# Performance work log

Measured on AMD Instinct MI355X. Metric: run time of the kernel, lower is better.

## Reference

```python
import jax, jax.numpy as jnp
import numpy as np

HEADS = 8
DIM_HEAD = 64
SCALE = DIM_HEAD ** -0.5

def layernorm_ch(x, g, eps=1e-5):
    # channel-wise LayerNorm over dim=1 (NCHW), biased variance
    mean = jnp.mean(x, axis=1, keepdims=True)
    var = jnp.var(x, axis=1, keepdims=True)
    return (x - mean) * jax.lax.rsqrt(var + eps) * g[None, :, None, None]

def setup_inputs() -> dict:
    key = jax.random.key(0)
    ks = jax.random.split(key, 4)
    B, C, H, W = 16, 512, 64, 64
    hidden = HEADS * DIM_HEAD
    x = jax.random.normal(ks[0], (B, C, H, W), dtype=jnp.float32)
    w_qkv = jax.random.normal(ks[1], (3 * hidden, C), dtype=jnp.float32) * (C ** -0.5)
    w_out = jax.random.normal(ks[2], (C, hidden), dtype=jnp.float32) * (hidden ** -0.5)
    b_out = jnp.zeros((C,), dtype=jnp.float32)
    g_out = jnp.ones((C,), dtype=jnp.float32)
    g_ln = jnp.ones((C,), dtype=jnp.float32)
    return {"x": x, "w_qkv": w_qkv, "w_out": w_out, "b_out": b_out, "g_out": g_out, "g_ln": g_ln}

def reference(x, w_qkv, w_out, b_out, g_out, g_ln):
    B, C, H, W = x.shape
    n = H * W
    x_norm = layernorm_ch(x, g_ln)
    # 1x1 conv == channel GEMM: [B,3*hidden,H,W]
    qkv = jnp.einsum('oc,bchw->bohw', w_qkv, x_norm)
    q, k, v = jnp.split(qkv, 3, axis=1)
    # b (h d) x y -> b h d n
    def to_heads(t):
        return t.reshape(B, HEADS, DIM_HEAD, n)
    q, k, v = to_heads(q), to_heads(k), to_heads(v)
    q = jax.nn.softmax(q, axis=-2) * SCALE   # softmax over d
    k = jax.nn.softmax(k, axis=-1)           # softmax over n
    v = v / n
    context = jnp.einsum('bhdn,bhen->bhde', k, v)
    out = jnp.einsum('bhde,bhdn->bhen', context, q)
    out = out.reshape(B, HEADS * DIM_HEAD, H, W)
    out = jnp.einsum('oc,bchw->bohw', w_out, out) + b_out[None, :, None, None]
    out = layernorm_ch(out, g_out)
    return out + x
```

## Files before the change

kernel.cpp:

```cpp
#include <hip/hip_runtime.h>
#include <math.h>

#define CCH    512
#define HWN    4096
#define NPIX   65536
#define OC3    1536
#define QSCALE 0.125f
#define LN_EPS 1e-5f

typedef _Float16 h16;
typedef h16  f16x8 __attribute__((ext_vector_type(8)));
typedef h16  f16x4 __attribute__((ext_vector_type(4)));
typedef float f32x4 __attribute__((ext_vector_type(4)));

__device__ __forceinline__ float waveReduceSum(float v) {
#pragma unroll
    for (int off = 32; off; off >>= 1) v += __shfl_xor(v, off);
    return v;
}

__device__ __forceinline__ void gl_lds16(const void* g, void* l) {
    __builtin_amdgcn_global_load_lds((const __attribute__((address_space(1))) void*)g,
                                     (__attribute__((address_space(3))) void*)l, 16, 0, 0);
}

__global__ __launch_bounds__(256) void transpose_prep(const float* __restrict__ src,
                                                      h16* __restrict__ dhi,
                                                      float* __restrict__ psum,
                                                      float* __restrict__ psq,
                                                      const float* __restrict__ w_qkv,
                                                      const float* __restrict__ g_ln,
                                                      const float* __restrict__ w_out,
                                                      h16* __restrict__ wg_h,
                                                      float* __restrict__ s,
                                                      h16* __restrict__ wo_h) {
    __shared__ float tile[64][65];
    __shared__ float ps1[4][64], ps2[4][64];
    const int t = threadIdx.x;

    if (blockIdx.z == 16) {
        const int o = (blockIdx.x + 64 * blockIdx.y) * 4 + (t >> 6);
        const int lane = t & 63;
        if (o < OC3) {
            float sum = 0.f;
#pragma unroll
            for (int j = 0; j < 8; ++j) {
                const int c = lane + j * 64;
                const float w = w_qkv[(size_t)o * CCH + c] * g_ln[c];
                wg_h[(size_t)o * CCH + c] = (h16)(w * 64.f);
                sum += w;
            }
            sum = waveReduceSum(sum);
            if (lane == 0) s[o] = sum;
        } else {
            const int r = o - OC3;
#pragma unroll
            for (int j = 0; j < 8; ++j) {
                const int c = lane + j * 64;
                wo_h[(size_t)r * CCH + c] = (h16)(w_out[(size_t)r * CCH + c] * 64.f);
            }
        }
        return;
    }

    const int b = blockIdx.z, c0 = blockIdx.y * 64, p0 = blockIdx.x * 64;
    const float* sb = src + ((size_t)b * CCH + c0) * HWN + p0;
    const int rc = t >> 4, cc4 = (t & 15) * 4;
#pragma unroll
    for (int ps = 0; ps < 4; ++ps) {
        const float4 v = *(const float4*)(sb + (size_t)(rc + ps * 16) * HWN + cc4);
        tile[rc + ps * 16][cc4 + 0] = v.x;
        tile[rc + ps * 16][cc4 + 1] = v.y;
        tile[rc + ps * 16][cc4 + 2] = v.z;
        tile[rc + ps * 16][cc4 + 3] = v.w;
    }
    __syncthreads();
    {
        const int q = t >> 6, px = t & 63;
        float s1 = 0.f, s2 = 0.f;
#pragma unroll
        for (int c = q * 16; c < q * 16 + 16; ++c) {
            const float v = tile[c][px];
            s1 += v; s2 += v * v;
        }
        ps1[q][px] = s1; ps2[q][px] = s2;
    }
    const int pr0 = t >> 3, cs = (t & 7) * 8;
#pragma unroll
    for (int ps = 0; ps < 2; ++ps) {
        const int pr = pr0 + ps * 32;
        f16x8 vh;
#pragma unroll
        for (int q = 0; q < 8; ++q) vh[q] = (h16)tile[cs + q][pr];
        const size_t o = ((size_t)b * HWN + p0 + pr) * CCH + c0 + cs;
        *(f16x8*)(dhi + o) = vh;
    }
    __syncthreads();
    if (t < 64) {
        const float s1 = ps1[0][t] + ps1[1][t] + ps1[2][t] + ps1[3][t];
        const float s2 = ps2[0][t] + ps2[1][t] + ps2[2][t] + ps2[3][t];
        const size_t gp = (size_t)b * HWN + p0 + t;
        psum[(size_t)(c0 >> 6) * NPIX + gp] = s1;
        psq [(size_t)(c0 >> 6) * NPIX + gp] = s2;
    }
}

__global__ __launch_bounds__(512) void qkv_gemm(const h16* __restrict__ Ahg,
                                                const h16* __restrict__ Bhg,
                                                const float* __restrict__ sv,
                                                const float* __restrict__ psum,
                                                const float* __restrict__ psq,
                                                h16* __restrict__ qout) {
    __shared__ __align__(16) h16 Ah[8192];
    __shared__ __align__(16) h16 Bh[16384];
    __shared__ float mnS[256], rsS[256];
    const int tid = threadIdx.x;
    const int om = blockIdx.x * 128;
    const int by0 = blockIdx.y;
    const int by  = (by0 & 7) * 32 + (by0 >> 3);
    const int p0  = by * 256;

    const int srow = tid >> 2;
    const int skh  = ((tid & 3) ^ (srow & 3)) * 8;
    const size_t a0 = (size_t)(om + srow) * CCH + skh;
    const size_t b0 = (size_t)(p0 + srow) * CCH + skh;

    const int lane = tid & 63;
    const int wv = tid >> 6;
    const int wm = (wv >> 2) * 64, wn = (wv & 3) * 64;
    const int lr = lane & 15, kg = lane >> 4;
    const int swz = (kg ^ (lr & 3)) * 8;

    f32x4 acc[4][4];
#pragma unroll
    for (int i = 0; i < 4; ++i)
#pragma unroll
        for (int j = 0; j < 4; ++j) acc[i][j] = {0.f, 0.f, 0.f, 0.f};

#define STAGE(KC)                                                          \
    do {                                                                   \
        gl_lds16(Ahg + a0 + (KC),                 Ah + tid * 8);           \
        gl_lds16(Ahg + a0 + (KC) + 32,            Ah + 4096 + tid * 8);    \
        gl_lds16(Bhg + b0 + (KC),                 Bh + tid * 8);           \
        gl_lds16(Bhg + b0 + (KC) + 128 * CCH,     Bh + 4096 + tid * 8);    \
        gl_lds16(Bhg + b0 + (KC) + 32,            Bh + 8192 + tid * 8);    \
        gl_lds16(Bhg + b0 + (KC) + 32 + 128 * CCH, Bh + 12288 + tid * 8);  \
    } while (0)

    STAGE(0);
    if (tid < 256) {
        const int gp = p0 + tid;
        float s1 = 0.f, s2 = 0.f;
#pragma unroll
        for (int cb = 0; cb < 8; ++cb) {
            s1 += psum[(size_t)cb * NPIX + gp];
            s2 += psq [(size_t)cb * NPIX + gp];
        }
        const float m = s1 * (1.f / 512.f);
        float var = s2 * (1.f / 512.f) - m * m;
        var = fmaxf(var, 0.f);
        mnS[tid] = m;
        rsS[tid] = rsqrtf(var + LN_EPS);
    }

#pragma unroll 1
    for (int kc = 0; kc < 512; kc += 64) {
        __syncthreads();
        f16x8 a0f[4], b0f[4], a1f[4], b1f[4];
#pragma unroll
        for (int i = 0; i < 4; ++i) {
            a0f[i] = *(const f16x8*)(Ah + (wm + i * 16 + lr) * 32 + swz);
            b0f[i] = *(const f16x8*)(Bh + (wn + i * 16 + lr) * 32 + swz);
        }
#pragma unroll
        for (int i = 0; i < 4; ++i)
#pragma unroll
            for (int j = 0; j < 4; ++j)
                acc[i][j] = __builtin_amdgcn_mfma_f32_16x16x32_f16(a0f[i], b0f[j], acc[i][j], 0, 0, 0);
#pragma unroll
        for (int i = 0; i < 4; ++i) {
            a1f[i] = *(const f16x8*)(Ah + 4096 + (wm + i * 16 + lr) * 32 + swz);
            b1f[i] = *(const f16x8*)(Bh + 8192 + (wn + i * 16 + lr) * 32 + swz);
        }
        __syncthreads();
        if (kc + 64 < 512) STAGE(kc + 64);
#pragma unroll
        for (int i = 0; i < 4; ++i)
#pragma unroll
            for (int j = 0; j < 4; ++j)
                acc[i][j] = __builtin_amdgcn_mfma_f32_16x16x32_f16(a1f[i], b1f[j], acc[i][j], 0, 0, 0);
    }
#undef STAGE

    const int b = p0 >> 12, hw0 = p0 & 4095;
    float mn[4], rs[4];
#pragma unroll
    for (int j = 0; j < 4; ++j) {
        const int px = wn + j * 16 + lr;
        mn[j] = mnS[px]; rs[j] = rsS[px];
    }
#pragma unroll
    for (int i = 0; i < 4; ++i)
#pragma unroll
        for (int r = 0; r < 4; ++r) {
            const int o = om + wm + i * 16 + kg * 4 + r;
            const float so = sv[o];
            h16* dst = qout + ((size_t)b * OC3 + o) * HWN;
#pragma unroll
            for (int j = 0; j < 4; ++j) {
                const int hw = hw0 + wn + j * 16 + lr;
                dst[hw] = (h16)(rs[j] * (acc[i][j][r] * (1.f / 64.f) - mn[j] * so));
            }
        }
}

__global__ __launch_bounds__(64) void ctx_partial(const h16* __restrict__ qkv16,
                                                  float* __restrict__ ctp) {
    const int bh = blockIdx.y, ci = blockIdx.x;
    const int b = bh >> 3, h = bh & 7;
    const h16* kb = qkv16 + ((size_t)b * OC3 + CCH  + h * 64) * HWN;
    const h16* vb = qkv16 + ((size_t)b * OC3 + 1024 + h * 64) * HWN;
    const int lane = threadIdx.x;
    const int lr = lane & 15, kg = lane >> 4;
    const int nbase = ci * 256 + kg * 8;

    float m[4] = {-1e30f, -1e30f, -1e30f, -1e30f};
#pragma unroll 1
    for (int c = 0; c < 8; ++c) {
        const int n0 = nbase + c * 32;
#pragma unroll
        for (int i = 0; i < 4; ++i) {
            const f16x8 kv = *(const f16x8*)(kb + (size_t)(i * 16 + lr) * HWN + n0);
#pragma unroll
            for (int u = 0; u < 8; ++u) m[i] = fmaxf(m[i], (float)kv[u]);
        }
    }
#pragma unroll
    for (int i = 0; i < 4; ++i) {
        m[i] = fmaxf(m[i], __shfl_xor(m[i], 16));
        m[i] = fmaxf(m[i], __shfl_xor(m[i], 32));
    }

    float z[4] = {0.f, 0.f, 0.f, 0.f};
    f32x4 acc[4][4];
#pragma unroll
    for (int i = 0; i < 4; ++i)
#pragma unroll
        for (int j = 0; j < 4; ++j) acc[i][j] = {0.f, 0.f, 0.f, 0.f};

#pragma unroll 1
    for (int c = 0; c < 8; ++c) {
        const int n0 = nbase + c * 32;
        f16x8 ke[4], vf[4];
#pragma unroll
        for (int j = 0; j < 4; ++j)
            vf[j] = *(const f16x8*)(vb + (size_t)(j * 16 + lr) * HWN + n0);
#pragma unroll
        for (int i = 0; i < 4; ++i) {
            const f16x8 kv = *(const f16x8*)(kb + (size_t)(i * 16 + lr) * HWN + n0);
            f16x8 t;
#pragma unroll
            for (int u = 0; u < 8; ++u) {
                const float e = __expf((float)kv[u] - m[i]);
                z[i] += e;
                t[u] = (h16)e;
            }
            ke[i] = t;
        }
#pragma unroll
        for (int i = 0; i < 4; ++i)
#pragma unroll
            for (int j = 0; j < 4; ++j)
                acc[i][j] = __builtin_amdgcn_mfma_f32_16x16x32_f16(ke[i], vf[j], acc[i][j], 0, 0, 0);
    }
#pragma unroll
    for (int i = 0; i < 4; ++i) {
        z[i] += __shfl_xor(z[i], 16);
        z[i] += __shfl_xor(z[i], 32);
    }
    float* dst = ctp + ((size_t)bh * 16 + ci) * 4224;
#pragma unroll
    for (int i = 0; i < 4; ++i)
#pragma unroll
        for (int j = 0; j < 4; ++j)
#pragma unroll
            for (int r = 0; r < 4; ++r)
                dst[(i * 16 + kg * 4 + r) * 64 + j * 16 + lr] = acc[i][j][r];
    if (kg == 0)
#pragma unroll
        for (int i = 0; i < 4; ++i) {
            dst[4096 + i * 16 + lr] = z[i];
            dst[4160 + i * 16 + lr] = m[i];
        }
}

__global__ __launch_bounds__(256) void ctx_reduce(const float* __restrict__ ctp,
                                                  h16* __restrict__ ctt) {
    __shared__ float w[16][64];
    __shared__ float rz[64];
    const int bh = blockIdx.x;
    const int tid = threadIdx.x;
    const float* src = ctp + (size_t)bh * 16 * 4224;
    if (tid < 64) {
        float M = -1e30f;
#pragma unroll
        for (int ci = 0; ci < 16; ++ci)
            M = fmaxf(M, src[(size_t)ci * 4224 + 4160 + tid]);
        float Z = 0.f;
#pragma unroll
        for (int ci = 0; ci < 16; ++ci) {
            const float ww = __expf(src[(size_t)ci * 4224 + 4160 + tid] - M);
            w[ci][tid] = ww;
            Z += ww * src[(size_t)ci * 4224 + 4096 + tid];
        }
        rz[tid] = 1.f / Z;
    }
    __syncthreads();
    h16* dstt = ctt + (size_t)bh * 4096;
    for (int e4 = tid * 4; e4 < 4096; e4 += 1024) {
        const int d = e4 >> 6, e0 = e4 & 63;
        float4 sum = make_float4(0.f, 0.f, 0.f, 0.f);
#pragma unroll
        for (int ci = 0; ci < 16; ++ci) {
            const float4 v = *(const float4*)(src + (size_t)ci * 4224 + e4);
            const float ww = w[ci][d];
            sum.x += ww * v.x; sum.y += ww * v.y;
            sum.z += ww * v.z; sum.w += ww * v.w;
        }
        const float r = rz[d];
        dstt[(e0 + 0) * 64 + d] = (h16)(sum.x * r);
        dstt[(e0 + 1) * 64 + d] = (h16)(sum.y * r);
        dstt[(e0 + 2) * 64 + d] = (h16)(sum.z * r);
        dstt[(e0 + 3) * 64 + d] = (h16)(sum.w * r);
    }
}

__global__ __launch_bounds__(256) void attn_out(const h16* __restrict__ qkv16,
                                                const h16* __restrict__ ctt,
                                                h16* __restrict__ at) {
    __shared__ __align__(16) h16 qt[64][72];

    const int bh = blockIdx.y, ci = blockIdx.x;
    const int b = bh >> 3, h = bh & 7;
    const h16* qb = qkv16 + ((size_t)b * OC3 + h * 64) * HWN;
    const int tid = threadIdx.x;
    const int lane = tid & 63, wv = tid >> 6;
    const int lr = lane & 15, kg = lane >> 4;

    const h16* cb = ctt + (size_t)bh * 4096 + (wv * 16 + lr) * 64 + kg * 8;
    f16x8 af0 = *(const f16x8*)(cb);
    f16x8 af1 = *(const f16x8*)(cb + 32);

    const int d  = tid >> 2;
    const int rn = tid >> 2, d0q = (tid & 3) * 16;

    for (int t = 0; t < 8; ++t) {
        const int n0 = ci * 512 + t * 64;
        __syncthreads();
#pragma unroll
        for (int jj = 0; jj < 2; ++jj) {
            const int nn = (tid & 3) * 8 + jj * 32;
            const f16x8 qv = *(const f16x8*)(qb + (size_t)d * HWN + n0 + nn);
#pragma unroll
            for (int u = 0; u < 8; ++u) qt[nn + u][d] = qv[u];
        }
        __syncthreads();
        {
            float qv[16];
            float mx = -1e30f;
#pragma unroll
            for (int dd = 0; dd < 16; ++dd) {
                qv[dd] = (float)qt[rn][d0q + dd];
                mx = fmaxf(mx, qv[dd]);
            }
            mx = fmaxf(mx, __shfl_xor(mx, 1));
            mx = fmaxf(mx, __shfl_xor(mx, 2));
            float sm = 0.f;
#pragma unroll
            for (int dd = 0; dd < 16; ++dd) {
                qv[dd] = __expf(qv[dd] - mx);
                sm += qv[dd];
            }
            sm += __shfl_xor(sm, 1);
            sm += __shfl_xor(sm, 2);
            const float sc = 512.f * QSCALE / sm;
#pragma unroll
            for (int dd = 0; dd < 16; ++dd)
                qt[rn][d0q + dd] = (h16)(qv[dd] * sc);
        }
        __syncthreads();
        f32x4 acc4[4];
#pragma unroll
        for (int j = 0; j < 4; ++j) acc4[j] = {0.f, 0.f, 0.f, 0.f};
#pragma unroll
        for (int j = 0; j < 4; ++j) {
            const f16x8 bf0 = *(const f16x8*)(&qt[j * 16 + lr][kg * 8]);
            const f16x8 bf1 = *(const f16x8*)(&qt[j * 16 + lr][32 + kg * 8]);
            acc4[j] = __builtin_amdgcn_mfma_f32_16x16x32_f16(af0, bf0, acc4[j], 0, 0, 0);
            acc4[j] = __builtin_amdgcn_mfma_f32_16x16x32_f16(af1, bf1, acc4[j], 0, 0, 0);
        }
        __syncthreads();
#pragma unroll
        for (int j = 0; j < 4; ++j) {
            f16x4 o4;
            o4[0] = (h16)acc4[j][0]; o4[1] = (h16)acc4[j][1];
            o4[2] = (h16)acc4[j][2]; o4[3] = (h16)acc4[j][3];
            *(f16x4*)(&qt[j * 16 + lr][wv * 16 + kg * 4]) = o4;
        }
        __syncthreads();
        {
            const int px = tid >> 2, e0 = (tid & 3) * 16;
            const f16x8 vh0 = *(const f16x8*)(&qt[px][e0]);
            const f16x8 vh1 = *(const f16x8*)(&qt[px][e0 + 8]);
            const size_t o = ((size_t)b * HWN + n0 + px) * CCH + h * 64 + e0;
            *(f16x8*)(at + o)     = vh0;
            *(f16x8*)(at + o + 8) = vh1;
        }
    }
}

__global__ __launch_bounds__(512) void out_fused(const h16* __restrict__ wo_hi,
                                                 const h16* __restrict__ at,
                                                 const float* __restrict__ b_out,
                                                 const float* __restrict__ g_out,
                                                 const float* __restrict__ x,
                                                 float* __restrict__ out) {
    __shared__ __align__(16) h16 Alds[512 * 32];
    __shared__ __align__(16) h16 Blds[128 * 32];
    __shared__ float red1[4][128], red2[4][128];
    __shared__ float mnS[128], rsS[128];

    const int tid = threadIdx.x;
    const int p0 = blockIdx.x * 128;
    const int b = p0 >> 12, hw0 = p0 & 4095;

    const int trow = tid >> 2;
    const int skh  = ((tid & 3) ^ (trow & 3)) * 8;
    const size_t aoff = (size_t)trow * CCH + skh;
    const size_t boff = (size_t)p0 * CCH + aoff;
    const int wofs = (tid >> 6) * 512;

    const int wv = tid >> 6;
    const int wm = (wv >> 1) * 128, wn = (wv & 1) * 64;
    const int lane = tid & 63;
    const int lr = lane & 15, kg = lane >> 4;
    const int swz = (kg ^ (lr & 3)) * 8;

    f32x4 acc[8][4];
#pragma unroll
    for (int i = 0; i < 8; ++i)
#pragma unroll
        for (int j = 0; j < 4; ++j) acc[i][j] = {0.f, 0.f, 0.f, 0.f};

#define STAGEF(S)                                                           \
    do {                                                                    \
        const int kc_ = (S) * 32;                                           \
        gl_lds16(wo_hi + aoff + kc_,               Alds + wofs);            \
        gl_lds16(wo_hi + aoff + kc_ + 128 * CCH,   Alds + 4096 + wofs);     \
        gl_lds16(wo_hi + aoff + kc_ + 256 * CCH,   Alds + 8192 + wofs);     \
        gl_lds16(wo_hi + aoff + kc_ + 384 * CCH,   Alds + 12288 + wofs);    \
        gl_lds16(at + boff + kc_,                  Blds + wofs);            \
    } while (0)

    STAGEF(0);
#pragma unroll 1
    for (int s = 0; s < 16; ++s) {
        __syncthreads();
        f16x8 af[8], bf[4];
#pragma unroll
        for (int i = 0; i < 8; ++i)
            af[i] = *(const f16x8*)(Alds + (wm + i * 16 + lr) * 32 + swz);
#pragma unroll
        for (int j = 0; j < 4; ++j)
            bf[j] = *(const f16x8*)(Blds + (wn + j * 16 + lr) * 32 + swz);
        __syncthreads();
        if (s < 15) STAGEF(s + 1);
#pragma unroll
        for (int i = 0; i < 8; ++i)
#pragma unroll
            for (int j = 0; j < 4; ++j)
                acc[i][j] = __builtin_amdgcn_mfma_f32_16x16x32_f16(af[i], bf[j], acc[i][j], 0, 0, 0);
    }
#undef STAGEF

#pragma unroll
    for (int i = 0; i < 8; ++i) {
        const int o = wm + i * 16 + kg * 4;
        const float4 bb = *(const float4*)(b_out + o);
#pragma unroll
        for (int j = 0; j < 4; ++j) {
            acc[i][j][0] = acc[i][j][0] * (1.f / 134217728.f) + bb.x;
            acc[i][j][1] = acc[i][j][1] * (1.f / 134217728.f) + bb.y;
            acc[i][j][2] = acc[i][j][2] * (1.f / 134217728.f) + bb.z;
            acc[i][j][3] = acc[i][j][3] * (1.f / 134217728.f) + bb.w;
        }
    }
    float s1[4], s2[4];
#pragma unroll
    for (int j = 0; j < 4; ++j) {
        s1[j] = 0.f; s2[j] = 0.f;
#pragma unroll
        for (int i = 0; i < 8; ++i)
#pragma unroll
            for (int r = 0; r < 4; ++r) {
                const float v = acc[i][j][r];
                s1[j] += v; s2[j] += v * v;
            }
        s1[j] += __shfl_xor(s1[j], 16); s1[j] += __shfl_xor(s1[j], 32);
        s2[j] += __shfl_xor(s2[j], 16); s2[j] += __shfl_xor(s2[j], 32);
    }
    if (kg == 0) {
#pragma unroll
        for (int j = 0; j < 4; ++j) {
            red1[wv >> 1][wn + j * 16 + lr] = s1[j];
            red2[wv >> 1][wn + j * 16 + lr] = s2[j];
        }
    }
    __syncthreads();
    if (tid < 128) {
        const float S1 = red1[0][tid] + red1[1][tid] + red1[2][tid] + red1[3][tid];
        const float S2 = red2[0][tid] + red2[1][tid] + red2[2][tid] + red2[3][tid];
        const float m = S1 * (1.f / 512.f);
        float var = S2 * (1.f / 512.f) - m * m;
        var = fmaxf(var, 0.f);
        mnS[tid] = m;
        rsS[tid] = rsqrtf(var + LN_EPS);
    }
    __syncthreads();
    float mj[4], rj[4];
#pragma unroll
    for (int j = 0; j < 4; ++j) {
        const int px = wn + j * 16 + lr;
        mj[j] = mnS[px]; rj[j] = rsS[px];
    }
#pragma unroll
    for (int i = 0; i < 8; ++i) {
        const int o = wm + i * 16 + kg * 4;
        const float4 gg = *(const float4*)(g_out + o);
#pragma unroll
        for (int r = 0; r < 4; ++r) {
            const float g = (r == 0) ? gg.x : (r == 1) ? gg.y : (r == 2) ? gg.z : gg.w;
            const float* xr = x + ((size_t)b * CCH + o + r) * HWN + hw0 + wn;
            float* dr = out + ((size_t)b * CCH + o + r) * HWN + hw0 + wn;
#pragma unroll
            for (int j = 0; j < 4; ++j) {
                const int c = j * 16 + lr;
                dr[c] = (acc[i][j][r] - mj[j]) * rj[j] * g + xr[c];
            }
        }
    }
}

extern "C" void kernel_launch(void* const* d_in, const int* in_sizes, int n_in,
                              void* d_out, int out_size, void* d_ws, size_t ws_size,
                              hipStream_t stream) {
    (void)in_sizes; (void)n_in; (void)out_size;
    const float* x     = (const float*)d_in[0];
    const float* w_qkv = (const float*)d_in[1];
    const float* w_out = (const float*)d_in[2];
    const float* b_out = (const float*)d_in[3];
    const float* g_out = (const float*)d_in[4];
    const float* g_ln  = (const float*)d_in[5];
    float* out = (float*)d_out;
    float* ws  = (float*)d_ws;

    float* s    = ws;
    h16*  ctt   = (h16*)(s + OC3);
    float* ctp  = s + OC3 + 524288;
    float* psum = ctp;
    float* psq  = psum + 524288;
    h16*  wg_hi = (h16*)(ctp + 8650752);
    h16*  wo_hi = wg_hi + 786432;
    h16*  qkv16 = wo_hi + 262144;
    h16*  at    = qkv16 + 100663296;
    h16*  xt_hi = (h16*)d_out;

    const size_t need = 76809728ULL * 4ULL;
    if (ws_size < need) return;

    transpose_prep<<<dim3(64, 8, 17), 256, 0, stream>>>(x, xt_hi, psum, psq,
                                                        w_qkv, g_ln, w_out,
                                                        wg_hi, s, wo_hi);
    qkv_gemm     <<<dim3(12, 256), 512, 0, stream>>>(wg_hi, xt_hi,
                                                     s, psum, psq, qkv16);
    ctx_partial  <<<dim3(16, 128), 64, 0, stream>>>(qkv16, ctp);
    ctx_reduce   <<<128, 256, 0, stream>>>(ctp, ctt);
    attn_out     <<<dim3(8, 128), 256, 0, stream>>>(qkv16, ctt, at);
    out_fused    <<<512, 512, 0, stream>>>(wo_hi, at,
                                           b_out, g_out, x, out);
}
```

Baseline: 384.8 us.

## Fuse attention-output (q softmax and context matmul) into the output projection GEMM

The separate attn_out kernel is removed. out_fused now computes the q softmax and the context×q product per head directly into shared memory, and uses that tile as the B operand of the w_out GEMM. This avoids writing and re-reading the 64 MB fp16 intermediate `at` and one kernel launch. In exchange, the per-head softmax and small MFMA work is serialized inside the GEMM loop with extra barriers, and the LDS footprint grows.

```diff
diff --git a/kernel.cpp b/kernel.cpp
--- a/kernel.cpp
+++ b/kernel.cpp
@@ -335,98 +335,15 @@
     }
 }
 
-__global__ __launch_bounds__(256) void attn_out(const h16* __restrict__ qkv16,
-                                                const h16* __restrict__ ctt,
-                                                h16* __restrict__ at) {
-    __shared__ __align__(16) h16 qt[64][72];
-
-    const int bh = blockIdx.y, ci = blockIdx.x;
-    const int b = bh >> 3, h = bh & 7;
-    const h16* qb = qkv16 + ((size_t)b * OC3 + h * 64) * HWN;
-    const int tid = threadIdx.x;
-    const int lane = tid & 63, wv = tid >> 6;
-    const int lr = lane & 15, kg = lane >> 4;
-
-    const h16* cb = ctt + (size_t)bh * 4096 + (wv * 16 + lr) * 64 + kg * 8;
-    f16x8 af0 = *(const f16x8*)(cb);
-    f16x8 af1 = *(const f16x8*)(cb + 32);
-
-    const int d  = tid >> 2;
-    const int rn = tid >> 2, d0q = (tid & 3) * 16;
-
-    for (int t = 0; t < 8; ++t) {
-        const int n0 = ci * 512 + t * 64;
-        __syncthreads();
-#pragma unroll
-        for (int jj = 0; jj < 2; ++jj) {
-            const int nn = (tid & 3) * 8 + jj * 32;
-            const f16x8 qv = *(const f16x8*)(qb + (size_t)d * HWN + n0 + nn);
-#pragma unroll
-            for (int u = 0; u < 8; ++u) qt[nn + u][d] = qv[u];
-        }
-        __syncthreads();
-        {
-            float qv[16];
-            float mx = -1e30f;
-#pragma unroll
-            for (int dd = 0; dd < 16; ++dd) {
-                qv[dd] = (float)qt[rn][d0q + dd];
-                mx = fmaxf(mx, qv[dd]);
-            }
-            mx = fmaxf(mx, __shfl_xor(mx, 1));
-            mx = fmaxf(mx, __shfl_xor(mx, 2));
-            float sm = 0.f;
-#pragma unroll
-            for (int dd = 0; dd < 16; ++dd) {
-                qv[dd] = __expf(qv[dd] - mx);
-                sm += qv[dd];
-            }
-            sm += __shfl_xor(sm, 1);
-            sm += __shfl_xor(sm, 2);
-            const float sc = 512.f * QSCALE / sm;
-#pragma unroll
-            for (int dd = 0; dd < 16; ++dd)
-                qt[rn][d0q + dd] = (h16)(qv[dd] * sc);
-        }
-        __syncthreads();
-        f32x4 acc4[4];
-#pragma unroll
-        for (int j = 0; j < 4; ++j) acc4[j] = {0.f, 0.f, 0.f, 0.f};
-#pragma unroll
-        for (int j = 0; j < 4; ++j) {
-            const f16x8 bf0 = *(const f16x8*)(&qt[j * 16 + lr][kg * 8]);
-            const f16x8 bf1 = *(const f16x8*)(&qt[j * 16 + lr][32 + kg * 8]);
-            acc4[j] = __builtin_amdgcn_mfma_f32_16x16x32_f16(af0, bf0, acc4[j], 0, 0, 0);
-            acc4[j] = __builtin_amdgcn_mfma_f32_16x16x32_f16(af1, bf1, acc4[j], 0, 0, 0);
-        }
-        __syncthreads();
-#pragma unroll
-        for (int j = 0; j < 4; ++j) {
-            f16x4 o4;
-            o4[0] = (h16)acc4[j][0]; o4[1] = (h16)acc4[j][1];
-            o4[2] = (h16)acc4[j][2]; o4[3] = (h16)acc4[j][3];
-            *(f16x4*)(&qt[j * 16 + lr][wv * 16 + kg * 4]) = o4;
-        }
-        __syncthreads();
-        {
-            const int px = tid >> 2, e0 = (tid & 3) * 16;
-            const f16x8 vh0 = *(const f16x8*)(&qt[px][e0]);
-            const f16x8 vh1 = *(const f16x8*)(&qt[px][e0 + 8]);
-            const size_t o = ((size_t)b * HWN + n0 + px) * CCH + h * 64 + e0;
-            *(f16x8*)(at + o)     = vh0;
-            *(f16x8*)(at + o + 8) = vh1;
-        }
-    }
-}
-
 __global__ __launch_bounds__(512) void out_fused(const h16* __restrict__ wo_hi,
-                                                 const h16* __restrict__ at,
+                                                 const h16* __restrict__ qkv16,
+                                                 const h16* __restrict__ ctt,
                                                  const float* __restrict__ b_out,
                                                  const float* __restrict__ g_out,
                                                  const float* __restrict__ x,
                                                  float* __restrict__ out) {
     __shared__ __align__(16) h16 Alds[512 * 32];
-    __shared__ __align__(16) h16 Blds[128 * 32];
+    __shared__ __align__(16) h16 qt[128][72];
     __shared__ float red1[4][128], red2[4][128];
     __shared__ float mnS[128], rsS[128];
 
@@ -437,14 +354,16 @@
     const int trow = tid >> 2;
     const int skh  = ((tid & 3) ^ (trow & 3)) * 8;
     const size_t aoff = (size_t)trow * CCH + skh;
-    const size_t boff = (size_t)p0 * CCH + aoff;
     const int wofs = (tid >> 6) * 512;
 
     const int wv = tid >> 6;
-    const int wm = (wv >> 1) * 128, wn = (wv & 1) * 64;
     const int lane = tid & 63;
     const int lr = lane & 15, kg = lane >> 4;
+    const int wm = (wv >> 1) * 128, wn = (wv & 1) * 64;
     const int swz = (kg ^ (lr & 3)) * 8;
+    const int pv_e0 = (wv & 3) * 16, pv_ph = (wv >> 2) * 64;
+    const int sm_px = tid >> 2, sm_d0 = (tid & 3) * 16;
+    const int ql_d = tid >> 3, ql_px = (tid & 7) * 16;
 
     f32x4 acc[8][4];
 #pragma unroll
@@ -459,27 +378,90 @@
         gl_lds16(wo_hi + aoff + kc_ + 128 * CCH,   Alds + 4096 + wofs);     \
         gl_lds16(wo_hi + aoff + kc_ + 256 * CCH,   Alds + 8192 + wofs);     \
         gl_lds16(wo_hi + aoff + kc_ + 384 * CCH,   Alds + 12288 + wofs);    \
-        gl_lds16(at + boff + kc_,                  Blds + wofs);            \
     } while (0)
 
     STAGEF(0);
+
 #pragma unroll 1
-    for (int s = 0; s < 16; ++s) {
+    for (int h = 0; h < 8; ++h) {
+        const h16* qb = qkv16 + ((size_t)b * OC3 + h * 64) * HWN + hw0;
+        {
+            const f16x8 q0 = *(const f16x8*)(qb + (size_t)ql_d * HWN + ql_px);
+            const f16x8 q1 = *(const f16x8*)(qb + (size_t)ql_d * HWN + ql_px + 8);
+#pragma unroll
+            for (int u = 0; u < 8; ++u) {
+                qt[ql_px + u][ql_d]     = q0[u];
+                qt[ql_px + 8 + u][ql_d] = q1[u];
+            }
+        }
         __syncthreads();
-        f16x8 af[8], bf[4];
-#pragma unroll
-        for (int i = 0; i < 8; ++i)
-            af[i] = *(const f16x8*)(Alds + (wm + i * 16 + lr) * 32 + swz);
-#pragma unroll
-        for (int j = 0; j < 4; ++j)
-            bf[j] = *(const f16x8*)(Blds + (wn + j * 16 + lr) * 32 + swz);
+        {
+            float qv[16];
+            float mx = -1e30f;
+#pragma unroll
+            for (int dd = 0; dd < 16; ++dd) {
+                qv[dd] = (float)qt[sm_px][sm_d0 + dd];
+                mx = fmaxf(mx, qv[dd]);
+            }
+            mx = fmaxf(mx, __shfl_xor(mx, 1));
+            mx = fmaxf(mx, __shfl_xor(mx, 2));
+            float sm = 0.f;
+#pragma unroll
+            for (int dd = 0; dd < 16; ++dd) {
+                qv[dd] = __expf(qv[dd] - mx);
+                sm += qv[dd];
+            }
+            sm += __shfl_xor(sm, 1);
+            sm += __shfl_xor(sm, 2);
+            const float sc = 512.f * QSCALE / sm;
+#pragma unroll
+            for (int dd = 0; dd < 16; ++dd)
+                qt[sm_px][sm_d0 + dd] = (h16)(qv[dd] * sc);
+        }
         __syncthreads();
-        if (s < 15) STAGEF(s + 1);
-#pragma unroll
-        for (int i = 0; i < 8; ++i)
+        {
+            const h16* cb = ctt + ((size_t)(b * 8 + h)) * 4096 + (pv_e0 + lr) * 64 + kg * 8;
+            const f16x8 af0 = *(const f16x8*)(cb);
+            const f16x8 af1 = *(const f16x8*)(cb + 32);
+            f32x4 acc4[4];
+#pragma unroll
+            for (int j = 0; j < 4; ++j) acc4[j] = {0.f, 0.f, 0.f, 0.f};
+#pragma unroll
+            for (int j = 0; j < 4; ++j) {
+                const int px = pv_ph + j * 16 + lr;
+                const f16x8 bf0 = *(const f16x8*)(&qt[px][kg * 8]);
+                const f16x8 bf1 = *(const f16x8*)(&qt[px][32 + kg * 8]);
+                acc4[j] = __builtin_amdgcn_mfma_f32_16x16x32_f16(af0, bf0, acc4[j], 0, 0, 0);
+                acc4[j] = __builtin_amdgcn_mfma_f32_16x16x32_f16(af1, bf1, acc4[j], 0, 0, 0);
+            }
+            __syncthreads();
+#pragma unroll
+            for (int j = 0; j < 4; ++j) {
+                f16x4 o4;
+                o4[0] = (h16)acc4[j][0]; o4[1] = (h16)acc4[j][1];
+                o4[2] = (h16)acc4[j][2]; o4[3] = (h16)acc4[j][3];
+                *(f16x4*)(&qt[pv_ph + j * 16 + lr][pv_e0 + kg * 4]) = o4;
+            }
+        }
+#pragma unroll 1
+        for (int ss = 0; ss < 2; ++ss) {
+            const int s = 2 * h + ss;
+            __syncthreads();
+            f16x8 af[8], bf[4];
+#pragma unroll
+            for (int i = 0; i < 8; ++i)
+                af[i] = *(const f16x8*)(Alds + (wm + i * 16 + lr) * 32 + swz);
 #pragma unroll
             for (int j = 0; j < 4; ++j)
-                acc[i][j] = __builtin_amdgcn_mfma_f32_16x16x32_f16(af[i], bf[j], acc[i][j], 0, 0, 0);
+                bf[j] = *(const f16x8*)(&qt[wn + j * 16 + lr][ss * 32 + kg * 8]);
+            __syncthreads();
+            if (s < 15) STAGEF(s + 1);
+#pragma unroll
+            for (int i = 0; i < 8; ++i)
+#pragma unroll
+                for (int j = 0; j < 4; ++j)
+                    acc[i][j] = __builtin_amdgcn_mfma_f32_16x16x32_f16(af[i], bf[j], acc[i][j], 0, 0, 0);
+        }
     }
 #undef STAGEF
 
@@ -572,10 +554,9 @@
     h16*  wg_hi = (h16*)(ctp + 8650752);
     h16*  wo_hi = wg_hi + 786432;
     h16*  qkv16 = wo_hi + 262144;
-    h16*  at    = qkv16 + 100663296;
     h16*  xt_hi = (h16*)d_out;
 
-    const size_t need = 76809728ULL * 4ULL;
+    const size_t need = 60032512ULL * 4ULL;
     if (ws_size < need) return;
 
     transpose_prep<<<dim3(64, 8, 17), 256, 0, stream>>>(x, xt_hi, psum, psq,
@@ -585,7 +566,6 @@
                                                      s, psum, psq, qkv16);
     ctx_partial  <<<dim3(16, 128), 64, 0, stream>>>(qkv16, ctp);
     ctx_reduce   <<<128, 256, 0, stream>>>(ctp, ctt);
-    attn_out     <<<dim3(8, 128), 256, 0, stream>>>(qkv16, ctt, at);
-    out_fused    <<<512, 512, 0, stream>>>(wo_hi, at,
+    out_fused    <<<512, 512, 0, stream>>>(wo_hi, qkv16, ctt,
                                            b_out, g_out, x, out);
 }
```

Result: faster. 377.0 us (median of 2 runs) (-2.0%).
